# Kernel optimization log

Hardware: AMD Instinct MI355X
Metric: run time of the kernel (lower is better)

## Reference

```python
import jax, jax.numpy as jnp
import numpy as np
import math

N = 65536
IN_FEATURES = 64
OUT_FEATURES = 64
N_MODES = 32
N_BASIS = 1 + 2 * N_MODES


def setup_inputs() -> dict:
    key = jax.random.key(0)
    k1, k2 = jax.random.split(key)
    x = jax.random.normal(k1, (N, IN_FEATURES), dtype=jnp.float32)
    coeffs = jax.random.normal(k2, (OUT_FEATURES, IN_FEATURES, N_BASIS), dtype=jnp.float32) * 0.1
    bias = jnp.zeros((OUT_FEATURES,), dtype=jnp.float32)
    return {"x": x, "coeffs": coeffs, "bias": bias}


def reference(x, coeffs, bias):
    # freqs: [modes] = (1..modes) * pi
    freqs = jnp.arange(1, N_MODES + 1, dtype=x.dtype) * jnp.asarray(math.pi, dtype=x.dtype)
    x_flat = x.reshape(-1, IN_FEATURES)                      # [n, i]
    angles = x_flat[..., None] * freqs                       # [n, i, m]
    ones = jnp.ones(x_flat.shape + (1,), dtype=x.dtype)      # [n, i, 1]
    basis = jnp.concatenate([ones, jnp.sin(angles), jnp.cos(angles)], axis=-1)  # [n, i, b]
    out = jnp.einsum('oib,nib->no', coeffs, basis) + bias    # [n, o]
    return out.reshape(*x.shape[:-1], OUT_FEATURES)
```

## Files before the change

### kernel.cpp

```cpp
#include <hip/hip_runtime.h>
#include <hip/hip_bf16.h>


typedef __bf16 bf16x8 __attribute__((ext_vector_type(8)));
typedef float  f32x4  __attribute__((ext_vector_type(4)));
typedef float  f32x16 __attribute__((ext_vector_type(16)));

#define PI_F 3.14159265358979323846f

__global__ __launch_bounds__(256) void fkan_repack(
    const float* __restrict__ coeffs, const float* __restrict__ bias,
    __bf16* __restrict__ Bp, float* __restrict__ bias2) {
  int gid  = blockIdx.x * 256 + threadIdx.x;
  int lane = gid & 63;
  int frag = gid >> 6;
  int m  = frag >> 4;
  int kc = (frag >> 1) & 7;
  int cc = frag & 1;
  int o  = cc * 32 + (lane & 31);
  int kq = lane >> 5;

  bf16x8 v;
  #pragma unroll
  for (int t = 0; t < 8; ++t) {
    int i = kc * 8 + kq * 4 + (t >> 1);
    int b = (t & 1) ? (33 + m) : (1 + m);
    v[t] = (__bf16)coeffs[(o * 64 + i) * 65 + b];
  }
  *(bf16x8*)(Bp + (size_t)frag * 512 + lane * 8) = v;

  if (blockIdx.x == 0 && threadIdx.x < 64) {
    int oo = threadIdx.x;
    float s = bias[oo];
    #pragma unroll 4
    for (int ii = 0; ii < 64; ++ii) s += coeffs[(oo * 64 + ii) * 65 + 0];
    bias2[oo] = s;
  }
}

__device__ __forceinline__ void stage_slice(const __bf16* __restrict__ Bp,
                                            __bf16* dst, int m, int wave,
                                            int lane) {
  const char* g = (const char*)Bp + (size_t)m * 16384 + wave * 4096 + lane * 16;
  char* l = (char*)dst + wave * 4096;
  #pragma unroll
  for (int r = 0; r < 4; ++r) {
    __builtin_amdgcn_global_load_lds(
        (const __attribute__((address_space(1))) void*)(g + r * 1024),
        (__attribute__((address_space(3))) void*)(l + r * 1024), 16, 0, 0);
  }
}

__global__ __launch_bounds__(256, 2) void fkan_main(
    const float* __restrict__ x, const __bf16* __restrict__ Bp,
    const float* __restrict__ bias2, float* __restrict__ out) {
  __shared__ __bf16 Bs[2][8192];

  int tid  = threadIdx.x;
  int wave = tid >> 6;
  int lane = tid & 63;
  int kq   = lane >> 5;
  int cl   = lane & 31;
  int row  = blockIdx.x * 128 + wave * 32 + cl;

  float T[32], sp[32], cp[32], sc[32], cc_[32];
  const float* xrow = x + (size_t)row * 64 + kq * 4;
  #pragma unroll
  for (int kc = 0; kc < 8; ++kc) {
    f32x4 v = *(const f32x4*)(xrow + kc * 8);
    #pragma unroll
    for (int e = 0; e < 4; ++e) {
      int p = kc * 4 + e;
      float ss, cs;
      __sincosf(PI_F * v[e], &ss, &cs);
      T[p] = 2.0f * cs;
      sc[p] = ss;  cc_[p] = cs;
      sp[p] = 0.f; cp[p] = 1.f;
    }
  }

  f32x16 acc[2];
  #pragma unroll
  for (int c2 = 0; c2 < 2; ++c2)
    #pragma unroll
    for (int r = 0; r < 16; ++r) acc[c2][r] = 0.f;

  stage_slice(Bp, &Bs[0][0], 0, wave, lane);
  __syncthreads();

  for (int m = 0; m < 32; m += 2) {
    if (m + 1 < 32) stage_slice(Bp, &Bs[1][0], m + 1, wave, lane);
    #pragma unroll
    for (int kc = 0; kc < 8; ++kc) {
      bf16x8 af;
      #pragma unroll
      for (int e = 0; e < 4; ++e) {
        af[2 * e]     = (__bf16)sc[kc * 4 + e];
        af[2 * e + 1] = (__bf16)cc_[kc * 4 + e];
      }
      #pragma unroll
      for (int c2 = 0; c2 < 2; ++c2) {
        bf16x8 bf = *(const bf16x8*)(&Bs[0][(kc * 2 + c2) * 512 + lane * 8]);
        acc[c2] = __builtin_amdgcn_mfma_f32_32x32x16_bf16(af, bf, acc[c2],
                                                          0, 0, 0);
      }
    }
    #pragma unroll
    for (int p = 0; p < 32; ++p) {
      sp[p] = fmaf(T[p], sc[p], -sp[p]);
      cp[p] = fmaf(T[p], cc_[p], -cp[p]);
    }
    __syncthreads();

    if (m + 2 < 32) stage_slice(Bp, &Bs[0][0], m + 2, wave, lane);
    #pragma unroll
    for (int kc = 0; kc < 8; ++kc) {
      bf16x8 af;
      #pragma unroll
      for (int e = 0; e < 4; ++e) {
        af[2 * e]     = (__bf16)sp[kc * 4 + e];
        af[2 * e + 1] = (__bf16)cp[kc * 4 + e];
      }
      #pragma unroll
      for (int c2 = 0; c2 < 2; ++c2) {
        bf16x8 bf = *(const bf16x8*)(&Bs[1][(kc * 2 + c2) * 512 + lane * 8]);
        acc[c2] = __builtin_amdgcn_mfma_f32_32x32x16_bf16(af, bf, acc[c2],
                                                          0, 0, 0);
      }
    }
    #pragma unroll
    for (int p = 0; p < 32; ++p) {
      sc[p]  = fmaf(T[p], sp[p], -sc[p]);
      cc_[p] = fmaf(T[p], cp[p], -cc_[p]);
    }
    __syncthreads();
  }

  float* orow = out + (size_t)(blockIdx.x * 128 + wave * 32) * 64;
  #pragma unroll
  for (int c2 = 0; c2 < 2; ++c2) {
    float b2 = bias2[c2 * 32 + cl];
    #pragma unroll
    for (int r = 0; r < 16; ++r) {
      int ro = (r & 3) + 8 * (r >> 2) + 4 * kq;
      orow[(size_t)ro * 64 + c2 * 32 + cl] = acc[c2][r] + b2;
    }
  }
}

extern "C" void kernel_launch(void* const* d_in, const int* in_sizes, int n_in,
                              void* d_out, int out_size, void* d_ws, size_t ws_size,
                              hipStream_t stream) {
  const float* x      = (const float*)d_in[0];
  const float* coeffs = (const float*)d_in[1];
  const float* bias   = (const float*)d_in[2];
  float* out = (float*)d_out;

  __bf16* Bp   = (__bf16*)d_ws;
  float* bias2 = (float*)((char*)d_ws + 512 * 1024);

  int n_rows = in_sizes[0] / 64;

  fkan_repack<<<128, 256, 0, stream>>>(coeffs, bias, Bp, bias2);
  fkan_main<<<n_rows / 128, 256, 0, stream>>>(x, Bp, bias2, out);
}
```

Before: 114.0 us.

## Double rows per wave, angle-addition recurrence, coalesced repack with atomic bias

```diff
diff --git a/kernel.cpp b/kernel.cpp
--- a/kernel.cpp
+++ b/kernel.cpp
@@ -9,33 +9,28 @@
 #define PI_F 3.14159265358979323846f
 
 __global__ __launch_bounds__(256) void fkan_repack(
-    const float* __restrict__ coeffs, const float* __restrict__ bias,
-    __bf16* __restrict__ Bp, float* __restrict__ bias2) {
-  int gid  = blockIdx.x * 256 + threadIdx.x;
-  int lane = gid & 63;
-  int frag = gid >> 6;
-  int m  = frag >> 4;
-  int kc = (frag >> 1) & 7;
-  int cc = frag & 1;
-  int o  = cc * 32 + (lane & 31);
-  int kq = lane >> 5;
-
-  bf16x8 v;
-  #pragma unroll
-  for (int t = 0; t < 8; ++t) {
-    int i = kc * 8 + kq * 4 + (t >> 1);
-    int b = (t & 1) ? (33 + m) : (1 + m);
-    v[t] = (__bf16)coeffs[(o * 64 + i) * 65 + b];
+    const float* __restrict__ coeffs, __bf16* __restrict__ Bp,
+    float* __restrict__ bias2sum) {
+  int gid = blockIdx.x * 256 + threadIdx.x;
+  if (gid >= 64 * 64 * 65) return;
+  float v = coeffs[gid];
+  int b  = gid % 65;
+  int oi = gid / 65;
+  int i = oi & 63;
+  int o = oi >> 6;
+  if (b == 0) {
+    atomicAdd(&bias2sum[o], v);
+    return;
   }
-  *(bf16x8*)(Bp + (size_t)frag * 512 + lane * 8) = v;
-
-  if (blockIdx.x == 0 && threadIdx.x < 64) {
-    int oo = threadIdx.x;
-    float s = bias[oo];
-    #pragma unroll 4
-    for (int ii = 0; ii < 64; ++ii) s += coeffs[(oo * 64 + ii) * 65 + 0];
-    bias2[oo] = s;
-  }
+  int m  = (b - 1) & 31;
+  int sc = (b >= 33) ? 1 : 0;
+  int kc = i >> 3;
+  int kq = (i >> 2) & 1;
+  int cc = o >> 5;
+  int frag = (m * 8 + kc) * 2 + cc;
+  int lane = kq * 32 + (o & 31);
+  int t = 2 * (i & 3) + sc;
+  Bp[frag * 512 + lane * 8 + t] = (__bf16)v;
 }
 
 __device__ __forceinline__ void stage_slice(const __bf16* __restrict__ Bp,
@@ -51,9 +46,10 @@
   }
 }
 
-__global__ __launch_bounds__(256, 2) void fkan_main(
+__global__ __launch_bounds__(256, 1) void fkan_main(
     const float* __restrict__ x, const __bf16* __restrict__ Bp,
-    const float* __restrict__ bias2, float* __restrict__ out) {
+    const float* __restrict__ bias, const float* __restrict__ bias2sum,
+    float* __restrict__ out) {
   __shared__ __bf16 Bs[2][8192];
 
   int tid  = threadIdx.x;
@@ -61,89 +57,83 @@
   int lane = tid & 63;
   int kq   = lane >> 5;
   int cl   = lane & 31;
-  int row  = blockIdx.x * 128 + wave * 32 + cl;
+  int rowbase = blockIdx.x * 256 + wave * 64;
 
-  float T[32], sp[32], cp[32], sc[32], cc_[32];
-  const float* xrow = x + (size_t)row * 64 + kq * 4;
+  float s1[64], c1[64], sm[64], cm[64];
   #pragma unroll
-  for (int kc = 0; kc < 8; ++kc) {
-    f32x4 v = *(const f32x4*)(xrow + kc * 8);
+  for (int t = 0; t < 2; ++t) {
+    const float* xrow = x + (size_t)(rowbase + t * 32 + cl) * 64 + kq * 4;
     #pragma unroll
-    for (int e = 0; e < 4; ++e) {
-      int p = kc * 4 + e;
-      float ss, cs;
-      __sincosf(PI_F * v[e], &ss, &cs);
-      T[p] = 2.0f * cs;
-      sc[p] = ss;  cc_[p] = cs;
-      sp[p] = 0.f; cp[p] = 1.f;
+    for (int kc = 0; kc < 8; ++kc) {
+      f32x4 v = *(const f32x4*)(xrow + kc * 8);
+      #pragma unroll
+      for (int e = 0; e < 4; ++e) {
+        int p = t * 32 + kc * 4 + e;
+        float ss, cs;
+        __sincosf(PI_F * v[e], &ss, &cs);
+        s1[p] = ss; c1[p] = cs;
+        sm[p] = ss; cm[p] = cs;
+      }
     }
   }
 
-  f32x16 acc[2];
+  f32x16 acc[2][2];
   #pragma unroll
-  for (int c2 = 0; c2 < 2; ++c2)
+  for (int t = 0; t < 2; ++t)
     #pragma unroll
-    for (int r = 0; r < 16; ++r) acc[c2][r] = 0.f;
+    for (int c2 = 0; c2 < 2; ++c2)
+      #pragma unroll
+      for (int r = 0; r < 16; ++r) acc[t][c2][r] = 0.f;
 
   stage_slice(Bp, &Bs[0][0], 0, wave, lane);
   __syncthreads();
 
-  for (int m = 0; m < 32; m += 2) {
-    if (m + 1 < 32) stage_slice(Bp, &Bs[1][0], m + 1, wave, lane);
+  for (int m = 0; m < 32; ++m) {
+    int buf = m & 1;
+    if (m < 31) stage_slice(Bp, &Bs[buf ^ 1][0], m + 1, wave, lane);
+
     #pragma unroll
     for (int kc = 0; kc < 8; ++kc) {
-      bf16x8 af;
+      bf16x8 af0, af1;
       #pragma unroll
       for (int e = 0; e < 4; ++e) {
-        af[2 * e]     = (__bf16)sc[kc * 4 + e];
-        af[2 * e + 1] = (__bf16)cc_[kc * 4 + e];
+        af0[2 * e]     = (__bf16)sm[kc * 4 + e];
+        af0[2 * e + 1] = (__bf16)cm[kc * 4 + e];
+        af1[2 * e]     = (__bf16)sm[32 + kc * 4 + e];
+        af1[2 * e + 1] = (__bf16)cm[32 + kc * 4 + e];
       }
       #pragma unroll
       for (int c2 = 0; c2 < 2; ++c2) {
-        bf16x8 bf = *(const bf16x8*)(&Bs[0][(kc * 2 + c2) * 512 + lane * 8]);
-        acc[c2] = __builtin_amdgcn_mfma_f32_32x32x16_bf16(af, bf, acc[c2],
-                                                          0, 0, 0);
+        bf16x8 bf = *(const bf16x8*)(&Bs[buf][(kc * 2 + c2) * 512 + lane * 8]);
+        acc[0][c2] = __builtin_amdgcn_mfma_f32_32x32x16_bf16(af0, bf,
+                                                             acc[0][c2], 0, 0, 0);
+        acc[1][c2] = __builtin_amdgcn_mfma_f32_32x32x16_bf16(af1, bf,
+                                                             acc[1][c2], 0, 0, 0);
       }
     }
-    #pragma unroll
-    for (int p = 0; p < 32; ++p) {
-      sp[p] = fmaf(T[p], sc[p], -sp[p]);
-      cp[p] = fmaf(T[p], cc_[p], -cp[p]);
-    }
-    __syncthreads();
 
-    if (m + 2 < 32) stage_slice(Bp, &Bs[0][0], m + 2, wave, lane);
-    #pragma unroll
-    for (int kc = 0; kc < 8; ++kc) {
-      bf16x8 af;
+    if (m < 31) {
       #pragma unroll
-      for (int e = 0; e < 4; ++e) {
-        af[2 * e]     = (__bf16)sp[kc * 4 + e];
-        af[2 * e + 1] = (__bf16)cp[kc * 4 + e];
+      for (int p = 0; p < 64; ++p) {
+        float t0 = sm[p];
+        sm[p] = fmaf(t0, c1[p],  cm[p] * s1[p]);
+        cm[p] = fmaf(cm[p], c1[p], -t0 * s1[p]);
       }
-      #pragma unroll
-      for (int c2 = 0; c2 < 2; ++c2) {
-        bf16x8 bf = *(const bf16x8*)(&Bs[1][(kc * 2 + c2) * 512 + lane * 8]);
-        acc[c2] = __builtin_amdgcn_mfma_f32_32x32x16_bf16(af, bf, acc[c2],
-                                                          0, 0, 0);
-      }
-    }
-    #pragma unroll
-    for (int p = 0; p < 32; ++p) {
-      sc[p]  = fmaf(T[p], sp[p], -sc[p]);
-      cc_[p] = fmaf(T[p], cp[p], -cc_[p]);
     }
     __syncthreads();
   }
 
-  float* orow = out + (size_t)(blockIdx.x * 128 + wave * 32) * 64;
   #pragma unroll
   for (int c2 = 0; c2 < 2; ++c2) {
-    float b2 = bias2[c2 * 32 + cl];
+    float bv = bias[c2 * 32 + cl] + bias2sum[c2 * 32 + cl];
     #pragma unroll
-    for (int r = 0; r < 16; ++r) {
-      int ro = (r & 3) + 8 * (r >> 2) + 4 * kq;
-      orow[(size_t)ro * 64 + c2 * 32 + cl] = acc[c2][r] + b2;
+    for (int t = 0; t < 2; ++t) {
+      float* orow = out + (size_t)(rowbase + t * 32) * 64;
+      #pragma unroll
+      for (int r = 0; r < 16; ++r) {
+        int ro = (r & 3) + 8 * (r >> 2) + 4 * kq;
+        orow[(size_t)ro * 64 + c2 * 32 + cl] = acc[t][c2][r] + bv;
+      }
     }
   }
 }
@@ -156,11 +146,13 @@
   const float* bias   = (const float*)d_in[2];
   float* out = (float*)d_out;
 
-  __bf16* Bp   = (__bf16*)d_ws;
-  float* bias2 = (float*)((char*)d_ws + 512 * 1024);
+  __bf16* Bp      = (__bf16*)d_ws;
+  float* bias2sum = (float*)((char*)d_ws + 512 * 1024);
 
   int n_rows = in_sizes[0] / 64;
 
-  fkan_repack<<<128, 256, 0, stream>>>(coeffs, bias, Bp, bias2);
-  fkan_main<<<n_rows / 128, 256, 0, stream>>>(x, Bp, bias2, out);
+  hipMemsetAsync(bias2sum, 0, 64 * sizeof(float), stream);
+  fkan_repack<<<(64 * 64 * 65 + 255) / 256, 256, 0, stream>>>(coeffs, Bp,
+                                                              bias2sum);
+  fkan_main<<<n_rows / 256, 256, 0, stream>>>(x, Bp, bias, bias2sum, out);
 }
```

Measured after the change: 140.1 us. 1.23x slower.
